# Kernel optimization log

Hardware: AMD Instinct MI355X
Metric: run time of the kernel (lower is better)

Reference implementation:

```python
import jax, jax.numpy as jnp
import numpy as np

DIM = 1024
HEADS = 16

def setup_inputs() -> dict:
    key = jax.random.key(0)
    ks = jax.random.split(key, 5)
    x = jax.random.normal(ks[0], (4, 2048, DIM), dtype=jnp.float32)
    s = 1.0 / np.sqrt(DIM)
    Wqkv = jax.random.normal(ks[1], (DIM, 3 * DIM), dtype=jnp.float32) * s
    bqkv = jnp.zeros((3 * DIM,), dtype=jnp.float32)
    Wproj = jax.random.normal(ks[2], (DIM, DIM), dtype=jnp.float32) * s
    bproj = jnp.zeros((DIM,), dtype=jnp.float32)
    return {"x": x, "Wqkv": Wqkv, "bqkv": bqkv, "Wproj": Wproj, "bproj": bproj}

def reference(x, Wqkv, bqkv, Wproj, bproj):
    B, N, D = x.shape
    H = HEADS
    hd = D // H
    scale = hd ** (-0.5)
    qkv = x @ Wqkv + bqkv                      # [B, N, 3D]
    q, k, v = jnp.split(qkv, 3, axis=-1)
    # [B, N, H, hd] -> [B, H, N, hd]
    q = q.reshape(B, N, H, hd).transpose(0, 2, 1, 3)
    k = k.reshape(B, N, H, hd).transpose(0, 2, 1, 3)
    v = v.reshape(B, N, H, hd).transpose(0, 2, 1, 3)
    attn = jnp.einsum('bhqd,bhkd->bhqk', q, k) * scale
    attn = jax.nn.softmax(attn, axis=-1)
    out = jnp.einsum('bhqk,bhkd->bhqd', attn, v)
    out = out.transpose(0, 2, 1, 3).reshape(B, N, D)
    return out @ Wproj + bproj
```

## Files before the change

kernel.cpp:

```cpp
#include <hip/hip_runtime.h>
#include <hip/hip_bf16.h>
#include <math.h>


typedef __bf16 bf16;
typedef __bf16 bf16x4 __attribute__((ext_vector_type(4)));
typedef __bf16 bf16x8 __attribute__((ext_vector_type(8)));
typedef float f32x4 __attribute__((ext_vector_type(4)));

#define AS1(p) ((const __attribute__((address_space(1))) void*)(p))
#define AS3(p) ((__attribute__((address_space(3))) void*)(p))

__device__ __forceinline__ void async16(const void* g, void* l) {
    __builtin_amdgcn_global_load_lds(AS1(g), AS3(l), 16, 0, 0);
}

#if __has_builtin(__builtin_amdgcn_exp2f)
#define EXP2(x) __builtin_amdgcn_exp2f(x)
#else
#define EXP2(x) exp2f(x)
#endif

#define QSCALE 0.18033688011112042f


__global__ __launch_bounds__(256) void prep(const float* __restrict__ x,
                                            bf16* __restrict__ xb,
                                            const float* __restrict__ Wqkv,
                                            bf16* __restrict__ wqkvt,
                                            const float* __restrict__ Wproj,
                                            bf16* __restrict__ wprojt) {
    __shared__ float t[32][33];
    const int bx = blockIdx.x;
    const int tid = threadIdx.x;

    if (bx < 8192) {
        const int i = bx * 256 + tid;
        float4 v = ((const float4*)x)[i];
        bf16x4 o;
        o.x = (bf16)v.x; o.y = (bf16)v.y; o.z = (bf16)v.z; o.w = (bf16)v.w;
        ((bf16x4*)xb)[i] = o;
        return;
    }

    const float* in;
    bf16* out;
    int N, n0, k0;
    if (bx < 11264) {
        const int b = bx - 8192;
        in = Wqkv; out = wqkvt; N = 3072;
        n0 = (b % 96) * 32; k0 = (b / 96) * 32;
    } else {
        const int b = bx - 11264;
        in = Wproj; out = wprojt; N = 1024;
        n0 = (b & 31) * 32; k0 = (b >> 5) * 32;
    }
    const int tx = tid & 31, ty = tid >> 5;
    #pragma unroll
    for (int j = 0; j < 32; j += 8)
        t[ty + j][tx] = in[(size_t)(k0 + ty + j) * N + n0 + tx];
    __syncthreads();
    #pragma unroll
    for (int j = 0; j < 32; j += 8)
        out[(size_t)(n0 + ty + j) * 1024 + k0 + tx] = (bf16)t[tx][ty + j];
}


#define GEMM_STAGE(B) do { \
    async16(ga0, la0_##B); async16(ga1, la1_##B); \
    async16(gb0, lb0_##B); async16(gb1, lb1_##B); \
    ga0 += 32; ga1 += 32; gb0 += 32; gb1 += 32; \
} while (0)

#define GEMM_COMPUTE(B) do { \
    bf16x8 af[4], bfr[4]; \
    _Pragma("unroll") \
    for (int i = 0; i < 4; i++) \
        af[i] = *(const bf16x8*)(As##B + (wm + i * 16 + c) * 32 + quad * 8); \
    _Pragma("unroll") \
    for (int j = 0; j < 4; j++) \
        bfr[j] = *(const bf16x8*)(Bs##B + (wn + j * 16 + c) * 32 + quad * 8); \
    _Pragma("unroll") \
    for (int i = 0; i < 4; i++) \
        _Pragma("unroll") \
        for (int j = 0; j < 4; j++) \
            acc[i][j] = __builtin_amdgcn_mfma_f32_16x16x32_bf16(af[i], bfr[j], acc[i][j], 0, 0, 0); \
} while (0)

__device__ __forceinline__ void gemm_mainloop(const bf16* __restrict__ A,
                                              const bf16* __restrict__ Bt,
                                              int K, int m0, int n0,
                                              bf16* As0, bf16* As1,
                                              bf16* Bs0, bf16* Bs1, f32x4 acc[4][4]) {
    const int tid = threadIdx.x;
    const int wave = tid >> 6, lane = tid & 63;
    const int c = lane & 15, quad = lane >> 4;
    const int wm = (wave & 1) * 64, wn = (wave >> 1) * 64;

    const int ci0 = (wave * 2 + 0) * 64 + lane;
    const int ci1 = (wave * 2 + 1) * 64 + lane;
    const bf16* ga0 = A  + (size_t)(m0 + (ci0 >> 2)) * K + (ci0 & 3) * 8;
    const bf16* ga1 = A  + (size_t)(m0 + (ci1 >> 2)) * K + (ci1 & 3) * 8;
    const bf16* gb0 = Bt + (size_t)(n0 + (ci0 >> 2)) * K + (ci0 & 3) * 8;
    const bf16* gb1 = Bt + (size_t)(n0 + (ci1 >> 2)) * K + (ci1 & 3) * 8;
    bf16* la0_0 = As0 + (wave * 2 + 0) * 512;
    bf16* la1_0 = As0 + (wave * 2 + 1) * 512;
    bf16* la0_1 = As1 + (wave * 2 + 0) * 512;
    bf16* la1_1 = As1 + (wave * 2 + 1) * 512;
    bf16* lb0_0 = Bs0 + (wave * 2 + 0) * 512;
    bf16* lb1_0 = Bs0 + (wave * 2 + 1) * 512;
    bf16* lb0_1 = Bs1 + (wave * 2 + 0) * 512;
    bf16* lb1_1 = Bs1 + (wave * 2 + 1) * 512;

    const int nIter = K >> 6;
    GEMM_STAGE(0);
    __syncthreads();
    for (int t = 0; t < nIter; t++) {
        GEMM_STAGE(1);
        GEMM_COMPUTE(0);
        __syncthreads();
        if (t < nIter - 1) GEMM_STAGE(0);
        GEMM_COMPUTE(1);
        __syncthreads();
    }
}


__global__ __launch_bounds__(256) void gemm_qkv(const bf16* __restrict__ A,
                                                const bf16* __restrict__ Bt,
                                                const float* __restrict__ bias,
                                                bf16* __restrict__ Qb,
                                                bf16* __restrict__ Kb,
                                                bf16* __restrict__ Vtb) {
    __shared__ __align__(16) bf16 As0[128 * 32];
    __shared__ __align__(16) bf16 As1[128 * 32];
    __shared__ __align__(16) bf16 Bs0[128 * 32];
    __shared__ __align__(16) bf16 Bs1[128 * 32];
    f32x4 acc[4][4] = {};
    const int m0 = blockIdx.x * 128, n0 = blockIdx.y * 128;
    gemm_mainloop(A, Bt, 1024, m0, n0, As0, As1, Bs0, Bs1, acc);

    const int tid = threadIdx.x;
    const int wave = tid >> 6, lane = tid & 63;
    const int c = lane & 15, quad = lane >> 4;
    const int wm = (wave & 1) * 64, wn = (wave >> 1) * 64;
    const int sel = n0 >> 10;
    bf16* QK = (sel == 0) ? Qb : Kb;
    const float qs = (sel == 0) ? QSCALE : 1.0f;

    #pragma unroll
    for (int j = 0; j < 4; j++) {
        const int nfull = n0 + wn + j * 16 + c;
        const int nmod = nfull & 1023;
        const int h = nmod >> 6, e = nmod & 63;
        const float bv = bias[nfull];
        #pragma unroll
        for (int i = 0; i < 4; i++) {
            const int mbase = m0 + wm + i * 16 + quad * 4;
            const int b = mbase >> 11, t = mbase & 2047;
            if (sel < 2) {
                bf16* dst = QK + (((size_t)(b * 16 + h) * 2048 + t) * 64 + e);
                #pragma unroll
                for (int r = 0; r < 4; r++)
                    dst[(size_t)r * 64] = (bf16)((acc[i][j][r] + bv) * qs);
            } else {
                bf16* dst = Vtb + ((size_t)(b * 16 + h) * 64 + e) * 2048 + t;
                bf16x4 v;
                v.x = (bf16)(acc[i][j][0] + bv);
                v.y = (bf16)(acc[i][j][1] + bv);
                v.z = (bf16)(acc[i][j][2] + bv);
                v.w = (bf16)(acc[i][j][3] + bv);
                *(bf16x4*)dst = v;
            }
        }
    }
}


#define ATTN_STAGE(B) do { \
    async16(kS0, kD0_##B); async16(kS1, kD1_##B); \
    async16(vS0, vD0_##B); async16(vS1, vD1_##B); \
    kS0 += 4096; kS1 += 4096; vS0 += 64; vS1 += 64; \
} while (0)

#define ATTN_COMPUTE(B) do { \
    _Pragma("unroll") \
    for (int j = 0; j < 4; j++) { \
        bf16x8 kf0 = *(const bf16x8*)(kb0_##B + j * 1024); \
        bf16x8 kf1 = *(const bf16x8*)(kb1_##B + j * 1024); \
        f32x4 s0 = {}, s1 = {}; \
        __builtin_amdgcn_s_setprio(1); \
        s0 = __builtin_amdgcn_mfma_f32_16x16x32_bf16(kf0, qf[0][0], s0, 0, 0, 0); \
        s0 = __builtin_amdgcn_mfma_f32_16x16x32_bf16(kf1, qf[0][1], s0, 0, 0, 0); \
        s1 = __builtin_amdgcn_mfma_f32_16x16x32_bf16(kf0, qf[1][0], s1, 0, 0, 0); \
        s1 = __builtin_amdgcn_mfma_f32_16x16x32_bf16(kf1, qf[1][1], s1, 0, 0, 0); \
        __builtin_amdgcn_s_setprio(0); \
        _Pragma("unroll") \
        for (int r = 0; r < 4; r++) { s0[r] = EXP2(s0[r]); s1[r] = EXP2(s1[r]); } \
        lsum[0] += s0; \
        lsum[1] += s1; \
        bf16x4 p0, p1; \
        p0.x = (bf16)s0[0]; p0.y = (bf16)s0[1]; p0.z = (bf16)s0[2]; p0.w = (bf16)s0[3]; \
        p1.x = (bf16)s1[0]; p1.y = (bf16)s1[1]; p1.z = (bf16)s1[2]; p1.w = (bf16)s1[3]; \
        *(bf16x4*)(pwa + j * 16) = p0; \
        *(bf16x4*)(pwb + j * 16) = p1; \
    } \
    _Pragma("unroll") \
    for (int gks = 0; gks < 2; gks++) { \
        const bf16* vbg = gks ? vb1_##B : vb0_##B; \
        bf16x8 vf[4]; \
        _Pragma("unroll") \
        for (int n2 = 0; n2 < 4; n2++) \
            vf[n2] = *(const bf16x8*)(vbg + n2 * 1024); \
        bf16x8 pf0 = *(const bf16x8*)(pra + gks * 32); \
        bf16x8 pf1 = *(const bf16x8*)(prb + gks * 32); \
        __builtin_amdgcn_s_setprio(1); \
        _Pragma("unroll") \
        for (int n2 = 0; n2 < 4; n2++) { \
            o[0][n2] = __builtin_amdgcn_mfma_f32_16x16x32_bf16(pf0, vf[n2], o[0][n2], 0, 0, 0); \
            o[1][n2] = __builtin_amdgcn_mfma_f32_16x16x32_bf16(pf1, vf[n2], o[1][n2], 0, 0, 0); \
        } \
        __builtin_amdgcn_s_setprio(0); \
    } \
} while (0)

__global__ __launch_bounds__(256, 3) void attn_kernel(const bf16* __restrict__ Q,
                                                      const bf16* __restrict__ Kg,
                                                      const bf16* __restrict__ Vt,
                                                      bf16* __restrict__ Out) {
    __shared__ __align__(16) bf16 Ks0[64 * 64];
    __shared__ __align__(16) bf16 Ks1[64 * 64];
    __shared__ __align__(16) bf16 Vs0[64 * 64];
    __shared__ __align__(16) bf16 Vs1[64 * 64];
    __shared__ __align__(16) bf16 Pl[4 * 2 * 16 * 72];

    const int bh = blockIdx.x, qt = blockIdx.y;
    const int tid = threadIdx.x;
    const int wave = tid >> 6, lane = tid & 63;
    const int c = lane & 15, quad = lane >> 4;

    const bf16* Qb = Q + (size_t)bh * 2048 * 64;
    bf16* pw = Pl + wave * 2304;

    const int qbase = qt * 128 + wave * 32;

    bf16x8 qf[2][2];
    #pragma unroll
    for (int i = 0; i < 2; i++)
        #pragma unroll
        for (int ks = 0; ks < 2; ks++)
            qf[i][ks] = *(const bf16x8*)(Qb + (size_t)(qbase + i * 16 + c) * 64 + ks * 32 + quad * 8);

    const int s0i = tid, s1i = 256 + tid;
    const int rk0 = s0i >> 3, cg0 = (s0i & 7) ^ (rk0 & 7);
    const int rk1 = s1i >> 3, cg1 = (s1i & 7) ^ (rk1 & 7);
    const bf16* kS0 = Kg + (size_t)bh * 2048 * 64 + rk0 * 64 + cg0 * 8;
    const bf16* kS1 = Kg + (size_t)bh * 2048 * 64 + rk1 * 64 + cg1 * 8;
    const bf16* vS0 = Vt + (size_t)bh * 64 * 2048 + (size_t)rk0 * 2048 + cg0 * 8;
    const bf16* vS1 = Vt + (size_t)bh * 64 * 2048 + (size_t)rk1 * 2048 + cg1 * 8;
    bf16* kD0_0 = Ks0 + (size_t)(wave * 64) * 8;
    bf16* kD1_0 = Ks0 + (size_t)(256 + wave * 64) * 8;
    bf16* kD0_1 = Ks1 + (size_t)(wave * 64) * 8;
    bf16* kD1_1 = Ks1 + (size_t)(256 + wave * 64) * 8;
    bf16* vD0_0 = Vs0 + (size_t)(wave * 64) * 8;
    bf16* vD1_0 = Vs0 + (size_t)(256 + wave * 64) * 8;
    bf16* vD0_1 = Vs1 + (size_t)(wave * 64) * 8;
    bf16* vD1_1 = Vs1 + (size_t)(256 + wave * 64) * 8;

    const int sw = c & 7;
    const int ch0 = (quad ^ sw) * 8, ch1 = ((quad ^ sw) ^ 4) * 8;
    const bf16* kb0_0 = Ks0 + c * 64 + ch0;
    const bf16* kb1_0 = Ks0 + c * 64 + ch1;
    const bf16* kb0_1 = Ks1 + c * 64 + ch0;
    const bf16* kb1_1 = Ks1 + c * 64 + ch1;
    const bf16* vb0_0 = Vs0 + c * 64 + ch0;
    const bf16* vb1_0 = Vs0 + c * 64 + ch1;
    const bf16* vb0_1 = Vs1 + c * 64 + ch0;
    const bf16* vb1_1 = Vs1 + c * 64 + ch1;
    bf16* pwa = pw + c * 72 + quad * 4;
    bf16* pwb = pwa + 16 * 72;
    const bf16* pra = pw + c * 72 + quad * 8;
    const bf16* prb = pra + 16 * 72;

    f32x4 lsum[2] = {};
    f32x4 o[2][4] = {};

    ATTN_STAGE(0);
    __syncthreads();
    for (int kv2 = 0; kv2 < 16; kv2++) {
        ATTN_STAGE(1);
        ATTN_COMPUTE(0);
        __syncthreads();
        if (kv2 < 15) ATTN_STAGE(0);
        ATTN_COMPUTE(1);
        __syncthreads();
    }

    const int b = bh >> 4, hh = bh & 15;
    #pragma unroll
    for (int i = 0; i < 2; i++) {
        float lh = (lsum[i][0] + lsum[i][1]) + (lsum[i][2] + lsum[i][3]);
        lh += __shfl_xor(lh, 16);
        lh += __shfl_xor(lh, 32);
        const float li0 = __shfl(lh, quad * 4 + 0);
        const float li1 = __shfl(lh, quad * 4 + 1);
        const float li2 = __shfl(lh, quad * 4 + 2);
        const float li3 = __shfl(lh, quad * 4 + 3);
        const float inv[4] = {1.f / li0, 1.f / li1, 1.f / li2, 1.f / li3};
        #pragma unroll
        for (int r = 0; r < 4; r++) {
            const int token = b * 2048 + qbase + i * 16 + quad * 4 + r;
            #pragma unroll
            for (int n2 = 0; n2 < 4; n2++) {
                const int feat = hh * 64 + n2 * 16 + c;
                Out[(size_t)token * 1024 + feat] = (bf16)(o[i][n2][r] * inv[r]);
            }
        }
    }
}


__global__ __launch_bounds__(256) void gemm_proj(const bf16* __restrict__ A,
                                                 const bf16* __restrict__ Bt,
                                                 const float* __restrict__ bias,
                                                 float* __restrict__ Out) {
    __shared__ __align__(16) bf16 As0[128 * 32];
    __shared__ __align__(16) bf16 As1[128 * 32];
    __shared__ __align__(16) bf16 Bs0[128 * 32];
    __shared__ __align__(16) bf16 Bs1[128 * 32];
    f32x4 acc[4][4] = {};
    const int m0 = blockIdx.x * 128, n0 = blockIdx.y * 128;
    gemm_mainloop(A, Bt, 1024, m0, n0, As0, As1, Bs0, Bs1, acc);

    const int tid = threadIdx.x;
    const int wave = tid >> 6, lane = tid & 63;
    const int c = lane & 15, quad = lane >> 4;
    const int wm = (wave & 1) * 64, wn = (wave >> 1) * 64;

    #pragma unroll
    for (int j = 0; j < 4; j++) {
        const int nn = n0 + wn + j * 16 + c;
        const float bv = bias[nn];
        #pragma unroll
        for (int i = 0; i < 4; i++) {
            const int m = m0 + wm + i * 16 + quad * 4;
            #pragma unroll
            for (int r = 0; r < 4; r++)
                Out[(size_t)(m + r) * 1024 + nn] = acc[i][j][r] + bv;
        }
    }
}


extern "C" void kernel_launch(void* const* d_in, const int* in_sizes, int n_in,
                              void* d_out, int out_size, void* d_ws, size_t ws_size,
                              hipStream_t stream) {
    const float* x     = (const float*)d_in[0];
    const float* Wqkv  = (const float*)d_in[1];
    const float* bqkv  = (const float*)d_in[2];
    const float* Wproj = (const float*)d_in[3];
    const float* bproj = (const float*)d_in[4];
    float* out = (float*)d_out;

    char* ws = (char*)d_ws;
    bf16* xb     = (bf16*)(ws);
    bf16* wqkvt  = (bf16*)(ws + 16777216);
    bf16* wprojt = (bf16*)(ws + 23068672);
    bf16* Qb     = (bf16*)(ws + 25165824);
    bf16* Kb     = (bf16*)(ws + 41943040);
    bf16* Vtb    = (bf16*)(ws + 58720256);
    bf16* attno  = xb;

    prep<<<12288, 256, 0, stream>>>(x, xb, Wqkv, wqkvt, Wproj, wprojt);
    gemm_qkv<<<dim3(64, 24), 256, 0, stream>>>(xb, wqkvt, bqkv, Qb, Kb, Vtb);
    attn_kernel<<<dim3(64, 16), 256, 0, stream>>>(Qb, Kb, Vtb, attno);
    gemm_proj<<<dim3(64, 8), 256, 0, stream>>>(attno, wprojt, bproj, out);
}
```

Measured before the change: 268.9 us.

## Triple-buffer GEMM mainloop with XOR-swizzled LDS and explicit waitcnt barriers

Moves the shared QKV/projection GEMM mainloop from double to triple buffering. Each stage is now guarded by an explicit vmcnt wait plus a barrier, so two async global-to-LDS loads stay in flight while MFMA compute runs. It also XOR-swizzles the 16-byte chunk layout in LDS to cut bank conflicts on fragment reads, and raises launch bounds to 3 blocks per CU. The trade-off is more LDS per block and an iteration count hard-coded for K=1024, which is fine only because both GEMMs use K=1024.

```diff
diff --git a/kernel.cpp b/kernel.cpp
--- a/kernel.cpp
+++ b/kernel.cpp
@@ -76,10 +76,10 @@
     bf16x8 af[4], bfr[4]; \
     _Pragma("unroll") \
     for (int i = 0; i < 4; i++) \
-        af[i] = *(const bf16x8*)(As##B + (wm + i * 16 + c) * 32 + quad * 8); \
+        af[i] = *(const bf16x8*)(pa_##B + (wm + i * 16) * 32); \
     _Pragma("unroll") \
     for (int j = 0; j < 4; j++) \
-        bfr[j] = *(const bf16x8*)(Bs##B + (wn + j * 16 + c) * 32 + quad * 8); \
+        bfr[j] = *(const bf16x8*)(pb_##B + (wn + j * 16) * 32); \
     _Pragma("unroll") \
     for (int i = 0; i < 4; i++) \
         _Pragma("unroll") \
@@ -87,11 +87,18 @@
             acc[i][j] = __builtin_amdgcn_mfma_f32_16x16x32_bf16(af[i], bfr[j], acc[i][j], 0, 0, 0); \
 } while (0)
 
+#define GEMM_SYNC(N) do { \
+    asm volatile("s_waitcnt vmcnt(" #N ") lgkmcnt(0)" ::: "memory"); \
+    __builtin_amdgcn_s_barrier(); \
+    __builtin_amdgcn_sched_barrier(0); \
+} while (0)
+
 __device__ __forceinline__ void gemm_mainloop(const bf16* __restrict__ A,
                                               const bf16* __restrict__ Bt,
                                               int K, int m0, int n0,
-                                              bf16* As0, bf16* As1,
-                                              bf16* Bs0, bf16* Bs1, f32x4 acc[4][4]) {
+                                              bf16* As0, bf16* As1, bf16* As2,
+                                              bf16* Bs0, bf16* Bs1, bf16* Bs2,
+                                              f32x4 acc[4][4]) {
     const int tid = threadIdx.x;
     const int wave = tid >> 6, lane = tid & 63;
     const int c = lane & 15, quad = lane >> 4;
@@ -99,46 +106,60 @@
 
     const int ci0 = (wave * 2 + 0) * 64 + lane;
     const int ci1 = (wave * 2 + 1) * 64 + lane;
-    const bf16* ga0 = A  + (size_t)(m0 + (ci0 >> 2)) * K + (ci0 & 3) * 8;
-    const bf16* ga1 = A  + (size_t)(m0 + (ci1 >> 2)) * K + (ci1 & 3) * 8;
-    const bf16* gb0 = Bt + (size_t)(n0 + (ci0 >> 2)) * K + (ci0 & 3) * 8;
-    const bf16* gb1 = Bt + (size_t)(n0 + (ci1 >> 2)) * K + (ci1 & 3) * 8;
+    const int cs0 = (ci0 & 3) ^ ((ci0 >> 3) & 3);
+    const int cs1 = (ci1 & 3) ^ ((ci1 >> 3) & 3);
+    const bf16* ga0 = A  + (size_t)(m0 + (ci0 >> 2)) * K + cs0 * 8;
+    const bf16* ga1 = A  + (size_t)(m0 + (ci1 >> 2)) * K + cs1 * 8;
+    const bf16* gb0 = Bt + (size_t)(n0 + (ci0 >> 2)) * K + cs0 * 8;
+    const bf16* gb1 = Bt + (size_t)(n0 + (ci1 >> 2)) * K + cs1 * 8;
     bf16* la0_0 = As0 + (wave * 2 + 0) * 512;
     bf16* la1_0 = As0 + (wave * 2 + 1) * 512;
     bf16* la0_1 = As1 + (wave * 2 + 0) * 512;
     bf16* la1_1 = As1 + (wave * 2 + 1) * 512;
+    bf16* la0_2 = As2 + (wave * 2 + 0) * 512;
+    bf16* la1_2 = As2 + (wave * 2 + 1) * 512;
     bf16* lb0_0 = Bs0 + (wave * 2 + 0) * 512;
     bf16* lb1_0 = Bs0 + (wave * 2 + 1) * 512;
     bf16* lb0_1 = Bs1 + (wave * 2 + 0) * 512;
     bf16* lb1_1 = Bs1 + (wave * 2 + 1) * 512;
-
-    const int nIter = K >> 6;
+    bf16* lb0_2 = Bs2 + (wave * 2 + 0) * 512;
+    bf16* lb1_2 = Bs2 + (wave * 2 + 1) * 512;
+
+    const int chs = (quad ^ ((c >> 1) & 3)) * 8;
+    const bf16* pa_0 = As0 + c * 32 + chs;
+    const bf16* pa_1 = As1 + c * 32 + chs;
+    const bf16* pa_2 = As2 + c * 32 + chs;
+    const bf16* pb_0 = Bs0 + c * 32 + chs;
+    const bf16* pb_1 = Bs1 + c * 32 + chs;
+    const bf16* pb_2 = Bs2 + c * 32 + chs;
+
     GEMM_STAGE(0);
-    __syncthreads();
-    for (int t = 0; t < nIter; t++) {
-        GEMM_STAGE(1);
-        GEMM_COMPUTE(0);
-        __syncthreads();
-        if (t < nIter - 1) GEMM_STAGE(0);
-        GEMM_COMPUTE(1);
-        __syncthreads();
-    }
-}
-
-
-__global__ __launch_bounds__(256) void gemm_qkv(const bf16* __restrict__ A,
-                                                const bf16* __restrict__ Bt,
-                                                const float* __restrict__ bias,
-                                                bf16* __restrict__ Qb,
-                                                bf16* __restrict__ Kb,
-                                                bf16* __restrict__ Vtb) {
+    GEMM_STAGE(1);
+    for (int t = 0; t < 10; t++) {
+        GEMM_SYNC(4); GEMM_STAGE(2); GEMM_COMPUTE(0);
+        GEMM_SYNC(4); GEMM_STAGE(0); GEMM_COMPUTE(1);
+        GEMM_SYNC(4); GEMM_STAGE(1); GEMM_COMPUTE(2);
+    }
+    GEMM_SYNC(4); GEMM_COMPUTE(0);
+    GEMM_SYNC(0); GEMM_COMPUTE(1);
+}
+
+
+__global__ __launch_bounds__(256, 3) void gemm_qkv(const bf16* __restrict__ A,
+                                                   const bf16* __restrict__ Bt,
+                                                   const float* __restrict__ bias,
+                                                   bf16* __restrict__ Qb,
+                                                   bf16* __restrict__ Kb,
+                                                   bf16* __restrict__ Vtb) {
     __shared__ __align__(16) bf16 As0[128 * 32];
     __shared__ __align__(16) bf16 As1[128 * 32];
+    __shared__ __align__(16) bf16 As2[128 * 32];
     __shared__ __align__(16) bf16 Bs0[128 * 32];
     __shared__ __align__(16) bf16 Bs1[128 * 32];
+    __shared__ __align__(16) bf16 Bs2[128 * 32];
     f32x4 acc[4][4] = {};
     const int m0 = blockIdx.x * 128, n0 = blockIdx.y * 128;
-    gemm_mainloop(A, Bt, 1024, m0, n0, As0, As1, Bs0, Bs1, acc);
+    gemm_mainloop(A, Bt, 1024, m0, n0, As0, As1, As2, Bs0, Bs1, Bs2, acc);
 
     const int tid = threadIdx.x;
     const int wave = tid >> 6, lane = tid & 63;
@@ -320,17 +341,19 @@
 }
 
 
-__global__ __launch_bounds__(256) void gemm_proj(const bf16* __restrict__ A,
-                                                 const bf16* __restrict__ Bt,
-                                                 const float* __restrict__ bias,
-                                                 float* __restrict__ Out) {
+__global__ __launch_bounds__(256, 3) void gemm_proj(const bf16* __restrict__ A,
+                                                    const bf16* __restrict__ Bt,
+                                                    const float* __restrict__ bias,
+                                                    float* __restrict__ Out) {
     __shared__ __align__(16) bf16 As0[128 * 32];
     __shared__ __align__(16) bf16 As1[128 * 32];
+    __shared__ __align__(16) bf16 As2[128 * 32];
     __shared__ __align__(16) bf16 Bs0[128 * 32];
     __shared__ __align__(16) bf16 Bs1[128 * 32];
+    __shared__ __align__(16) bf16 Bs2[128 * 32];
     f32x4 acc[4][4] = {};
     const int m0 = blockIdx.x * 128, n0 = blockIdx.y * 128;
-    gemm_mainloop(A, Bt, 1024, m0, n0, As0, As1, Bs0, Bs1, acc);
+    gemm_mainloop(A, Bt, 1024, m0, n0, As0, As1, As2, Bs0, Bs1, Bs2, acc);
 
     const int tid = threadIdx.x;
     const int wave = tid >> 6, lane = tid & 63;
```

Result: faster. 258.6 us (-3.8%).
